# Kernel tuning notes

Measured on AMD Instinct MI355X. Metric: run time of the kernel, lower is better.

Reference implementation:

```python
import jax, jax.numpy as jnp
import numpy as np

K = 31      # avg_pool2d kernel
PAD = 15    # padding; PyTorch avg_pool2d default count_include_pad=True -> divide by K*K always


def _avg_pool_31(t):
    # windowed sum with zero padding, then fixed divisor K*K (count_include_pad=True)
    s = jax.lax.reduce_window(
        t, 0.0, jax.lax.add,
        window_dimensions=(1, 1, K, K),
        window_strides=(1, 1, 1, 1),
        padding=[(0, 0), (0, 0), (PAD, PAD), (PAD, PAD)],
    )
    return s / (K * K)


def setup_inputs() -> dict:
    key = jax.random.key(0)
    k1, k2 = jax.random.split(key)
    logits = jax.random.normal(k1, (32, 1, 512, 512), dtype=jnp.float32)
    targets = jax.random.uniform(k2, (32, 1, 512, 512), dtype=jnp.float32)
    return {"logits": logits, "targets": targets}


def reference(logits, targets):
    B = targets.shape[0]
    weight = 1.0 + 5.0 * jnp.abs(_avg_pool_31(targets) - targets)
    # numerically stable BCE-with-logits, reduction='none'
    bce = jnp.maximum(logits, 0.0) - logits * targets + jnp.log1p(jnp.exp(-jnp.abs(logits)))
    w = weight.reshape(B, -1)
    num = (w * bce.reshape(B, -1)).sum(axis=1)
    den = w.sum(axis=1)
    return (num / den).sum() / B
```

## Files before the change

kernel.cpp:

```cpp
#include <hip/hip_runtime.h>
#include <math.h>

#define BATCH 32
#define H 512
#define W 512
#define PAD 15
#define BAND 8
#define NBANDS (H / BAND)
#define NBLOCKS (BATCH * NBANDS)
#define NXCD 8
#define INV_KK (1.0f / 961.0f)

#define EMIT(tv, lv, hs)                                                      \
    {                                                                         \
        float pooled_ = (hs) * INV_KK;                                        \
        float wgt_ = fmaf(5.f, fabsf(pooled_ - (tv)), 1.f);                   \
        float al_ = fabsf(lv);                                                \
        float bce_ = fmaxf((lv), 0.f) - (lv) * (tv)                           \
                     + __logf(1.f + __expf(-al_));                            \
        num = fmaf(wgt_, bce_, num);                                          \
        den += wgt_;                                                          \
    }

#define KSLOT(pk, pkm1, tv, lv, FIRST, LAST)                                  \
    {                                                                         \
        float hs_ = base_;                                                    \
        if (!(LAST)) {                                                        \
            float sa_ = __shfl_up(tot_ - (pk), 2);                            \
            hs_ += okm2 ? sa_ : 0.f;                                          \
        }                                                                     \
        if (!(FIRST)) {                                                       \
            float se_ = __shfl_down((pkm1), 2);                               \
            hs_ += okp2 ? se_ : 0.f;                                          \
        }                                                                     \
        EMIT(tv, lv, hs_)                                                     \
    }

#define ROW_EMIT(va, vb, t0_, t1_, l0_, l1_)                                  \
    {                                                                         \
        const float p0_ = (va).x;                                             \
        const float p1_ = p0_ + (va).y;                                       \
        const float p2_ = p1_ + (va).z;                                       \
        const float p3_ = p2_ + (va).w;                                       \
        const float p4_ = p3_ + (vb).x;                                       \
        const float p5_ = p4_ + (vb).y;                                       \
        const float p6_ = p5_ + (vb).z;                                       \
        const float tot_ = p6_ + (vb).w;                                      \
        const float bm_ = __shfl_up(tot_, 1);                                 \
        const float dp_ = __shfl_down(tot_, 1);                               \
        const float base_ = (okm1 ? bm_ : 0.f) + tot_ + (okp1 ? dp_ : 0.f);   \
        KSLOT(p0_, 0.f, (t0_).x, (l0_).x, 1, 0)                               \
        KSLOT(p1_, p0_, (t0_).y, (l0_).y, 0, 0)                               \
        KSLOT(p2_, p1_, (t0_).z, (l0_).z, 0, 0)                               \
        KSLOT(p3_, p2_, (t0_).w, (l0_).w, 0, 0)                               \
        KSLOT(p4_, p3_, (t1_).x, (l1_).x, 0, 0)                               \
        KSLOT(p5_, p4_, (t1_).y, (l1_).y, 0, 0)                               \
        KSLOT(p6_, p5_, (t1_).z, (l1_).z, 0, 0)                               \
        KSLOT(0.f, p6_, (t1_).w, (l1_).w, 0, 1)                               \
    }

#define LDG(pa, pb, ptr, yy)                                                  \
    { const float4* p_ = (const float4*)((ptr) + (size_t)(yy) * W + x0);      \
      pa = p_[0]; pb = p_[1]; }

#define P1_INIT(G, C0, C1)                                                    \
    _Pragma("unroll")                                                         \
    for (int c = (C0); c < (C1); ++c) {                                       \
        const int y = y0 + c - PAD;                                           \
        float a0 = 0.f, a1 = 0.f;                                             \
        if ((G) || (unsigned)y < (unsigned)H) {                               \
            a0 = tcol[y * W]; a1 = tcol[y * W + 256];                         \
        }                                                                     \
        run0 += a0; run1 += a1;                                               \
    }

#define P1_SLIDE(G, J0, J1)                                                   \
    _Pragma("unroll")                                                         \
    for (int j = (J0); j < (J1); ++j) {                                       \
        vs[j][tid] = run0; vs[j][tid + 256] = run1;                           \
        if (j < BAND - 1) {                                                   \
            const int ye = y0 + j + PAD + 1, yl = y0 + j - PAD;               \
            float e0 = 0.f, e1 = 0.f, s0 = 0.f, s1 = 0.f;                     \
            if ((G) || (unsigned)ye < (unsigned)H) {                          \
                e0 = tcol[ye * W]; e1 = tcol[ye * W + 256];                   \
            }                                                                 \
            if ((G) || (unsigned)yl < (unsigned)H) {                          \
                s0 = tcol[yl * W]; s1 = tcol[yl * W + 256];                   \
            }                                                                 \
            run0 += e0 - s0; run1 += e1 - s1;                                 \
        }                                                                     \
    }

#define PHASE1(G)                                                             \
    P1_INIT(G, 0, 8)   __builtin_amdgcn_sched_barrier(0);                     \
    P1_INIT(G, 8, 16)  __builtin_amdgcn_sched_barrier(0);                     \
    P1_INIT(G, 16, 24) __builtin_amdgcn_sched_barrier(0);                     \
    P1_INIT(G, 24, 31)                                                        \
    P1_SLIDE(G, 0, 4)  __builtin_amdgcn_sched_barrier(0);                     \
    P1_SLIDE(G, 4, 8)

__global__ __launch_bounds__(256)
void wbce_band_kernel(const float* __restrict__ logits,
                      const float* __restrict__ targets,
                      float* __restrict__ partials) {
    __shared__ __align__(16) float vs[BAND][W];
    __shared__ float rn[4], rd[4];

    const int tid  = threadIdx.x;
    const int lane = tid & 63;
    const int w    = tid >> 6;

    const int bid  = (int)blockIdx.x;
    const int sbid = (bid & (NXCD - 1)) * (NBLOCKS / NXCD) + (bid >> 3);

    const int img  = sbid >> 6;
    const int band = sbid & (NBANDS - 1);
    const int y0   = band * BAND;
    const int x0   = lane * 8;

    const float* tb = targets + (size_t)img * H * W;
    const float* lb = logits  + (size_t)img * H * W;
    const float* tcol = tb + tid;

    const int jw = w * 2;
    float4 T0a, T0b, T1a, T1b, L0a, L0b, L1a, L1b;
    LDG(T0a, T0b, tb, y0 + jw + 0) LDG(L0a, L0b, lb, y0 + jw + 0)
    LDG(T1a, T1b, tb, y0 + jw + 1) LDG(L1a, L1b, lb, y0 + jw + 1)
    __builtin_amdgcn_sched_barrier(0);

    float run0 = 0.f, run1 = 0.f;
    if (y0 >= PAD && y0 + BAND + PAD - 1 < H) {
        PHASE1(1)
    } else {
        PHASE1(0)
    }
    __syncthreads();

    const bool okm2 = lane >= 2, okm1 = lane >= 1;
    const bool okp1 = lane <= 62, okp2 = lane <= 61;
    float num = 0.f, den = 0.f;

    {
        float4 A0 = ((const float4*)vs[jw + 0])[2 * lane];
        float4 B0 = ((const float4*)vs[jw + 0])[2 * lane + 1];
        float4 A1 = ((const float4*)vs[jw + 1])[2 * lane];
        float4 B1 = ((const float4*)vs[jw + 1])[2 * lane + 1];
        ROW_EMIT(A0, B0, T0a, T0b, L0a, L0b)
        ROW_EMIT(A1, B1, T1a, T1b, L1a, L1b)
    }

    #pragma unroll
    for (int off = 32; off > 0; off >>= 1) {
        num += __shfl_down(num, off);
        den += __shfl_down(den, off);
    }
    if (lane == 0) { rn[w] = num; rd[w] = den; }
    __syncthreads();
    if (tid == 0) {
        float n = 0.f, d = 0.f;
        #pragma unroll
        for (int i = 0; i < 4; ++i) { n += rn[i]; d += rd[i]; }
        partials[sbid * 2]     = n;
        partials[sbid * 2 + 1] = d;
    }
}

__global__ __launch_bounds__(1024)
void wbce_finalize_kernel(const float* __restrict__ partials,
                          float* __restrict__ out) {
    __shared__ float rsum[16];
    const int t = threadIdx.x;
    const int img = t >> 5;
    const int j = t & 31;
    const int base = img * NBANDS;
    float num = partials[(base + j) * 2]     + partials[(base + 32 + j) * 2];
    float den = partials[(base + j) * 2 + 1] + partials[(base + 32 + j) * 2 + 1];
    #pragma unroll
    for (int off = 16; off > 0; off >>= 1) {
        num += __shfl_down(num, off, 32);
        den += __shfl_down(den, off, 32);
    }
    float ratio = 0.f;
    if ((t & 31) == 0) ratio = num / den;
    ratio += __shfl_down(ratio, 32);
    const int lane = t & 63;
    const int wv = t >> 6;
    if (lane == 0) rsum[wv] = ratio;
    __syncthreads();
    if (t == 0) {
        float s = 0.f;
        #pragma unroll
        for (int i = 0; i < 16; ++i) s += rsum[i];
        out[0] = s / (float)BATCH;
    }
}

extern "C" void kernel_launch(void* const* d_in, const int* in_sizes, int n_in,
                              void* d_out, int out_size, void* d_ws, size_t ws_size,
                              hipStream_t stream) {
    const float* logits  = (const float*)d_in[0];
    const float* targets = (const float*)d_in[1];
    float* out = (float*)d_out;
    float* partials = (float*)d_ws;

    wbce_band_kernel<<<NBLOCKS, 256, 0, stream>>>(logits, targets, partials);
    wbce_finalize_kernel<<<1, 1024, 0, stream>>>(partials, out);
}
```

Measured before the change: 25.29 us.

## Defer row loads past phase 1, drop block reduction, raise occupancy hint

Moves the per-row target and logit global loads from kernel start into the row pass after the shared-memory vertical sums, shortening register live ranges. Adds a waves-per-EU occupancy attribute and splits the phase-1 init loop into smaller scheduling groups. Removes the second __syncthreads and shared cross-wave reduction by writing per-wave partials, so the finalize kernel now sums 8 values per thread. The risk is exposing global load latency that was previously overlapped with phase 1, plus four times as many partials to write and read.

```diff
diff --git a/kernel.cpp b/kernel.cpp
--- a/kernel.cpp
+++ b/kernel.cpp
@@ -36,32 +36,36 @@
         EMIT(tv, lv, hs_)                                                     \
     }
 
-#define ROW_EMIT(va, vb, t0_, t1_, l0_, l1_)                                  \
+#define LDG(pa, pb, ptr, yy)                                                  \
+    { const float4* p_ = (const float4*)((ptr) + (size_t)(yy) * W + x0);      \
+      pa = p_[0]; pb = p_[1]; }
+
+#define ROWPASS(r)                                                            \
     {                                                                         \
-        const float p0_ = (va).x;                                             \
-        const float p1_ = p0_ + (va).y;                                       \
-        const float p2_ = p1_ + (va).z;                                       \
-        const float p3_ = p2_ + (va).w;                                       \
-        const float p4_ = p3_ + (vb).x;                                       \
-        const float p5_ = p4_ + (vb).y;                                       \
-        const float p6_ = p5_ + (vb).z;                                       \
-        const float tot_ = p6_ + (vb).w;                                      \
+        float4 A_ = ((const float4*)vs[(r)])[2 * lane];                       \
+        float4 B_ = ((const float4*)vs[(r)])[2 * lane + 1];                   \
+        float4 Ta_, Tb_, La_, Lb_;                                            \
+        LDG(Ta_, Tb_, tb, y0 + (r)) LDG(La_, Lb_, lb, y0 + (r))               \
+        const float p0_ = A_.x;                                               \
+        const float p1_ = p0_ + A_.y;                                         \
+        const float p2_ = p1_ + A_.z;                                         \
+        const float p3_ = p2_ + A_.w;                                         \
+        const float p4_ = p3_ + B_.x;                                         \
+        const float p5_ = p4_ + B_.y;                                         \
+        const float p6_ = p5_ + B_.z;                                         \
+        const float tot_ = p6_ + B_.w;                                        \
         const float bm_ = __shfl_up(tot_, 1);                                 \
         const float dp_ = __shfl_down(tot_, 1);                               \
         const float base_ = (okm1 ? bm_ : 0.f) + tot_ + (okp1 ? dp_ : 0.f);   \
-        KSLOT(p0_, 0.f, (t0_).x, (l0_).x, 1, 0)                               \
-        KSLOT(p1_, p0_, (t0_).y, (l0_).y, 0, 0)                               \
-        KSLOT(p2_, p1_, (t0_).z, (l0_).z, 0, 0)                               \
-        KSLOT(p3_, p2_, (t0_).w, (l0_).w, 0, 0)                               \
-        KSLOT(p4_, p3_, (t1_).x, (l1_).x, 0, 0)                               \
-        KSLOT(p5_, p4_, (t1_).y, (l1_).y, 0, 0)                               \
-        KSLOT(p6_, p5_, (t1_).z, (l1_).z, 0, 0)                               \
-        KSLOT(0.f, p6_, (t1_).w, (l1_).w, 0, 1)                               \
-    }
-
-#define LDG(pa, pb, ptr, yy)                                                  \
-    { const float4* p_ = (const float4*)((ptr) + (size_t)(yy) * W + x0);      \
-      pa = p_[0]; pb = p_[1]; }
+        KSLOT(p0_, 0.f, Ta_.x, La_.x, 1, 0)                                   \
+        KSLOT(p1_, p0_, Ta_.y, La_.y, 0, 0)                                   \
+        KSLOT(p2_, p1_, Ta_.z, La_.z, 0, 0)                                   \
+        KSLOT(p3_, p2_, Ta_.w, La_.w, 0, 0)                                   \
+        KSLOT(p4_, p3_, Tb_.x, Lb_.x, 0, 0)                                   \
+        KSLOT(p5_, p4_, Tb_.y, Lb_.y, 0, 0)                                   \
+        KSLOT(p6_, p5_, Tb_.z, Lb_.z, 0, 0)                                   \
+        KSLOT(0.f, p6_, Tb_.w, Lb_.w, 0, 1)                                   \
+    }
 
 #define P1_INIT(G, C0, C1)                                                    \
     _Pragma("unroll")                                                         \
@@ -92,19 +96,23 @@
     }
 
 #define PHASE1(G)                                                             \
-    P1_INIT(G, 0, 8)   __builtin_amdgcn_sched_barrier(0);                     \
-    P1_INIT(G, 8, 16)  __builtin_amdgcn_sched_barrier(0);                     \
-    P1_INIT(G, 16, 24) __builtin_amdgcn_sched_barrier(0);                     \
-    P1_INIT(G, 24, 31)                                                        \
+    P1_INIT(G, 0, 4)   __builtin_amdgcn_sched_barrier(0);                     \
+    P1_INIT(G, 4, 8)   __builtin_amdgcn_sched_barrier(0);                     \
+    P1_INIT(G, 8, 12)  __builtin_amdgcn_sched_barrier(0);                     \
+    P1_INIT(G, 12, 16) __builtin_amdgcn_sched_barrier(0);                     \
+    P1_INIT(G, 16, 20) __builtin_amdgcn_sched_barrier(0);                     \
+    P1_INIT(G, 20, 24) __builtin_amdgcn_sched_barrier(0);                     \
+    P1_INIT(G, 24, 28) __builtin_amdgcn_sched_barrier(0);                     \
+    P1_INIT(G, 28, 31) __builtin_amdgcn_sched_barrier(0);                     \
     P1_SLIDE(G, 0, 4)  __builtin_amdgcn_sched_barrier(0);                     \
     P1_SLIDE(G, 4, 8)
 
 __global__ __launch_bounds__(256)
+__attribute__((amdgpu_waves_per_eu(8)))
 void wbce_band_kernel(const float* __restrict__ logits,
                       const float* __restrict__ targets,
                       float* __restrict__ partials) {
     __shared__ __align__(16) float vs[BAND][W];
-    __shared__ float rn[4], rd[4];
 
     const int tid  = threadIdx.x;
     const int lane = tid & 63;
@@ -121,12 +129,6 @@
     const float* tb = targets + (size_t)img * H * W;
     const float* lb = logits  + (size_t)img * H * W;
     const float* tcol = tb + tid;
-
-    const int jw = w * 2;
-    float4 T0a, T0b, T1a, T1b, L0a, L0b, L1a, L1b;
-    LDG(T0a, T0b, tb, y0 + jw + 0) LDG(L0a, L0b, lb, y0 + jw + 0)
-    LDG(T1a, T1b, tb, y0 + jw + 1) LDG(L1a, L1b, lb, y0 + jw + 1)
-    __builtin_amdgcn_sched_barrier(0);
 
     float run0 = 0.f, run1 = 0.f;
     if (y0 >= PAD && y0 + BAND + PAD - 1 < H) {
@@ -140,28 +142,19 @@
     const bool okp1 = lane <= 62, okp2 = lane <= 61;
     float num = 0.f, den = 0.f;
 
-    {
-        float4 A0 = ((const float4*)vs[jw + 0])[2 * lane];
-        float4 B0 = ((const float4*)vs[jw + 0])[2 * lane + 1];
-        float4 A1 = ((const float4*)vs[jw + 1])[2 * lane];
-        float4 B1 = ((const float4*)vs[jw + 1])[2 * lane + 1];
-        ROW_EMIT(A0, B0, T0a, T0b, L0a, L0b)
-        ROW_EMIT(A1, B1, T1a, T1b, L1a, L1b)
-    }
+    const int jw = w * 2;
+    ROWPASS(jw)
+    ROWPASS(jw + 1)
 
     #pragma unroll
     for (int off = 32; off > 0; off >>= 1) {
         num += __shfl_down(num, off);
         den += __shfl_down(den, off);
     }
-    if (lane == 0) { rn[w] = num; rd[w] = den; }
-    __syncthreads();
-    if (tid == 0) {
-        float n = 0.f, d = 0.f;
-        #pragma unroll
-        for (int i = 0; i < 4; ++i) { n += rn[i]; d += rd[i]; }
-        partials[sbid * 2]     = n;
-        partials[sbid * 2 + 1] = d;
+    if (lane == 0) {
+        const int wid = sbid * 4 + w;
+        partials[wid * 2]     = num;
+        partials[wid * 2 + 1] = den;
     }
 }
 
@@ -172,9 +165,13 @@
     const int t = threadIdx.x;
     const int img = t >> 5;
     const int j = t & 31;
-    const int base = img * NBANDS;
-    float num = partials[(base + j) * 2]     + partials[(base + 32 + j) * 2];
-    float den = partials[(base + j) * 2 + 1] + partials[(base + 32 + j) * 2 + 1];
+    const int base = img * 256;
+    float num = 0.f, den = 0.f;
+    #pragma unroll
+    for (int k = 0; k < 8; ++k) {
+        num += partials[(base + j + 32 * k) * 2];
+        den += partials[(base + j + 32 * k) * 2 + 1];
+    }
     #pragma unroll
     for (int off = 16; off > 0; off >>= 1) {
         num += __shfl_down(num, off, 32);
```

After: 26.44 us. 1.05x slower.
